# Optimization experiments

Hardware: AMD Instinct MI355X
Metric: run time of the kernel (lower is better)

## Reference

```python
import jax, jax.numpy as jnp
import numpy as np

B, T, DIM, H = 4, 2048, 512, 8
DECAY = 0.9

def setup_inputs():
    key = jax.random.key(0)
    ks = jax.random.split(key, 8)
    s = 1.0 / np.sqrt(DIM)
    def lin(k):
        return jax.random.normal(k, (DIM, DIM), jnp.float32) * s
    return {
        "q": jax.random.normal(ks[0], (B, T, DIM), jnp.float32),
        "k": jax.random.normal(ks[1], (B, T, DIM), jnp.float32),
        "v": jax.random.normal(ks[2], (B, T, DIM), jnp.float32),
        "Wa": lin(ks[3]), "ba": jnp.zeros((DIM,), jnp.float32),
        "Wb": lin(ks[4]), "bb": jnp.zeros((DIM,), jnp.float32),
        "Wg": lin(ks[5]), "bg": jnp.zeros((DIM,), jnp.float32),
        "Wo": lin(ks[6]), "bo": jnp.zeros((DIM,), jnp.float32),
    }

def _linear_scan(a, b):
    # h_t = a_t * h_{t-1} + b_t along time axis=1, via associative scan
    def combine(c1, c2):
        a1, b1 = c1
        a2, b2 = c2
        return a1 * a2, a2 * b1 + b2
    return jax.lax.associative_scan(combine, (a, b), axis=1)[1]

def reference(q, k, v, Wa, ba, Wb, bb, Wg, bg, Wo, bo):
    # --- Mamba-style selective scan on q (no residual) ---
    a = jax.nn.sigmoid(q @ Wa + ba)   # input-dependent decay [B,T,D]
    b = q @ Wb + bb                   # input injection       [B,T,D]
    h = _linear_scan(a, b)            # recurrent state       [B,T,D]
    g = jax.nn.sigmoid(q @ Wg + bg)   # gate
    m_out = (h * g) @ Wo + bo         # [B,T,D]

    # --- RetNet-style decay-weighted linear retention ---
    Dh = DIM // H
    qh = q.reshape(B, T, H, Dh)
    kh = k.reshape(B, T, H, Dh)
    vh = v.reshape(B, T, H, Dh)
    t = jnp.arange(T)
    delta = t[:, None] - t[None, :]           # t - s
    mask = delta >= 0                         # causal
    decay_mat = jnp.where(
        mask,
        jnp.exp(jnp.where(mask, delta, 0).astype(jnp.float32) * np.float32(np.log(DECAY))),
        0.0,
    )                                          # [T,T]
    scores = jnp.einsum('bthd,bshd->bhts', qh, kh) * decay_mat  # [B,H,T,T]
    r_out = jnp.einsum('bhts,bshd->bthd', scores, vh).reshape(B, T, DIM)

    return m_out + r_out
```

## Files before the change

kernel.cpp:

```cpp
#include <hip/hip_runtime.h>
#include <hip/hip_bf16.h>

typedef unsigned short u16;

#define BB 4
#define TT 2048
#define DIM 512
#define NH 8
#define DH 64
#define DECAY 0.9f

#define CC 64
#define NC 32
#define BHN 32

#define CHS 32
#define NSC 64

#define TM 128
#define TN 128
#define BK 64

#define SS 72

typedef __attribute__((ext_vector_type(8))) short bf16x8;
typedef __attribute__((ext_vector_type(4))) float f32x4;

__device__ __forceinline__ u16 f2bfu(float f) {
  union { float f; unsigned int u; } c; c.f = f;
  unsigned int u = c.u + 0x7FFFu + ((c.u >> 16) & 1u);
  return (u16)(u >> 16);
}
__device__ __forceinline__ float bf2f(u16 u) {
  union { unsigned int u; float f; } c; c.u = ((unsigned int)u) << 16;
  return c.f;
}

__device__ __forceinline__ void gl_lds16(const void* g, void* l) {
  __builtin_amdgcn_global_load_lds(
      (const __attribute__((address_space(1))) void*)g,
      (__attribute__((address_space(3))) void*)(unsigned int)(unsigned long long)l,
      16, 0, 0);
}

__device__ __forceinline__ void gemm_tile(
    int nTile, int mTile, const u16* __restrict__ A, const u16* __restrict__ Bt,
    const float* __restrict__ b0, const float* __restrict__ b1,
    const float* __restrict__ b2,
    u16* __restrict__ C0, u16* __restrict__ C1, u16* __restrict__ C2,
    int act_mask, u16* As, u16* Bs, int tid) {
  int wave = tid >> 6, lane = tid & 63;
  int group = (nTile * TN) >> 9;
  const float* bias = (group == 0) ? b0 : (group == 1) ? b1 : b2;
  u16* C = (group == 0) ? C0 : (group == 1) ? C1 : C2;
  int act = (act_mask >> group) & 1;

  int wm = (wave >> 1) * 64, wn = (wave & 1) * 64;
  int rowA = lane & 15, khalf = lane >> 4;

  f32x4 acc[4][4];
#pragma unroll
  for (int i = 0; i < 4; ++i)
#pragma unroll
    for (int j = 0; j < 4; ++j) acc[i][j] = (f32x4){0.f, 0.f, 0.f, 0.f};

  const u16* Abase = A + (size_t)mTile * TM * 512;
  const u16* Bbase = Bt + (size_t)nTile * TN * 512;

  for (int kk = 0; kk < 512; kk += BK) {
#pragma unroll
    for (int i = 0; i < 4; ++i) {
      int o = (wave * 4 + i) * 64 + lane;
      int row = o >> 3, gk = (o & 7) ^ (row & 7);
      gl_lds16(Abase + (size_t)row * 512 + kk + gk * 8, &As[o * 8]);
    }
#pragma unroll
    for (int i = 0; i < 4; ++i) {
      int o = (wave * 4 + i) * 64 + lane;
      int row = o >> 3, gk = (o & 7) ^ (row & 7);
      gl_lds16(Bbase + (size_t)row * 512 + kk + gk * 8, &Bs[o * 8]);
    }
    __syncthreads();
#pragma unroll
    for (int k0 = 0; k0 < 2; ++k0) {
      bf16x8 af[4], bfr[4];
#pragma unroll
      for (int mi = 0; mi < 4; ++mi) {
        int rr = wm + mi * 16 + rowA;
        int gk = k0 * 4 + khalf;
        int o = rr * 8 + (gk ^ (rr & 7));
        af[mi] = *(const bf16x8*)&As[o * 8];
      }
#pragma unroll
      for (int ni = 0; ni < 4; ++ni) {
        int rr = wn + ni * 16 + rowA;
        int gk = k0 * 4 + khalf;
        int o = rr * 8 + (gk ^ (rr & 7));
        bfr[ni] = *(const bf16x8*)&Bs[o * 8];
      }
#pragma unroll
      for (int mi = 0; mi < 4; ++mi)
#pragma unroll
        for (int ni = 0; ni < 4; ++ni)
          acc[mi][ni] = __builtin_amdgcn_mfma_f32_16x16x32_bf16(
              af[mi], bfr[ni], acc[mi][ni], 0, 0, 0);
    }
    __syncthreads();
  }
  int cloc = lane & 15, rq = (lane >> 4) * 4;
#pragma unroll
  for (int mi = 0; mi < 4; ++mi) {
#pragma unroll
    for (int r = 0; r < 4; ++r) {
      int m = mTile * TM + wm + mi * 16 + rq + r;
#pragma unroll
      for (int ni = 0; ni < 4; ++ni) {
        int n = (nTile * TN + wn + ni * 16 + cloc) & 511;
        float vv = acc[mi][ni][r] + bias[n];
        if (act) vv = 1.0f / (1.0f + __expf(-vv));
        C[(size_t)m * 512 + n] = f2bfu(vv);
      }
    }
  }
}

__device__ __forceinline__ void gemm_tile64(
    int nTile, int mTile, const u16* __restrict__ A, const u16* __restrict__ Bt,
    const float* __restrict__ bias, float* __restrict__ C,
    const u16* __restrict__ Radd, u16* As, u16* Bs, int tid) {
  int wave = tid >> 6, lane = tid & 63;
  int wm = wave * 32;
  int rowA = lane & 15, khalf = lane >> 4;

  f32x4 acc[2][4];
#pragma unroll
  for (int i = 0; i < 2; ++i)
#pragma unroll
    for (int j = 0; j < 4; ++j) acc[i][j] = (f32x4){0.f, 0.f, 0.f, 0.f};

  const u16* Abase = A + (size_t)mTile * TM * 512;
  const u16* Bbase = Bt + (size_t)nTile * 64 * 512;

  for (int kk = 0; kk < 512; kk += BK) {
#pragma unroll
    for (int i = 0; i < 4; ++i) {
      int o = (wave * 4 + i) * 64 + lane;
      int row = o >> 3, gk = (o & 7) ^ (row & 7);
      gl_lds16(Abase + (size_t)row * 512 + kk + gk * 8, &As[o * 8]);
    }
#pragma unroll
    for (int i = 0; i < 2; ++i) {
      int o = (wave * 2 + i) * 64 + lane;
      int row = o >> 3, gk = (o & 7) ^ (row & 7);
      gl_lds16(Bbase + (size_t)row * 512 + kk + gk * 8, &Bs[o * 8]);
    }
    __syncthreads();
#pragma unroll
    for (int k0 = 0; k0 < 2; ++k0) {
      bf16x8 af[2], bfr[4];
#pragma unroll
      for (int mi = 0; mi < 2; ++mi) {
        int rr = wm + mi * 16 + rowA;
        int gk = k0 * 4 + khalf;
        int o = rr * 8 + (gk ^ (rr & 7));
        af[mi] = *(const bf16x8*)&As[o * 8];
      }
#pragma unroll
      for (int ni = 0; ni < 4; ++ni) {
        int rr = ni * 16 + rowA;
        int gk = k0 * 4 + khalf;
        int o = rr * 8 + (gk ^ (rr & 7));
        bfr[ni] = *(const bf16x8*)&Bs[o * 8];
      }
#pragma unroll
      for (int mi = 0; mi < 2; ++mi)
#pragma unroll
        for (int ni = 0; ni < 4; ++ni)
          acc[mi][ni] = __builtin_amdgcn_mfma_f32_16x16x32_bf16(
              af[mi], bfr[ni], acc[mi][ni], 0, 0, 0);
    }
    __syncthreads();
  }
  int cloc = lane & 15, rq = (lane >> 4) * 4;
#pragma unroll
  for (int mi = 0; mi < 2; ++mi) {
#pragma unroll
    for (int r = 0; r < 4; ++r) {
      int m = mTile * TM + wm + mi * 16 + rq + r;
#pragma unroll
      for (int ni = 0; ni < 4; ++ni) {
        int n = nTile * 64 + ni * 16 + cloc;
        float vv = acc[mi][ni][r] + bias[n] + bf2f(Radd[(size_t)m * 512 + n]);
        C[(size_t)m * 512 + n] = vv;
      }
    }
  }
}

__global__ __launch_bounds__(256) void k1_prep(
    const float* __restrict__ q, u16* __restrict__ qbf,
    const float* __restrict__ W0, const float* __restrict__ W1,
    const float* __restrict__ W2, const float* __restrict__ W3,
    u16* __restrict__ Wt) {
  __shared__ float t[32][33];
  int bx = blockIdx.x, tid = threadIdx.x;
  if (bx < 1024) {
    int m = bx >> 8, rem = bx & 255;
    int n0 = (rem & 15) * 32, k0 = (rem >> 4) * 32;
    const float* W = (m == 0) ? W0 : (m == 1) ? W1 : (m == 2) ? W2 : W3;
    int tx = tid & 31, ty = tid >> 5;
#pragma unroll
    for (int r = 0; r < 32; r += 8)
      t[ty + r][tx] = W[(size_t)(k0 + ty + r) * DIM + n0 + tx];
    __syncthreads();
    u16* o = Wt + (size_t)m * DIM * DIM;
#pragma unroll
    for (int r = 0; r < 32; r += 8)
      o[(size_t)(n0 + ty + r) * DIM + k0 + tx] = f2bfu(t[tx][ty + r]);
  } else {
    int i = (bx - 1024) * 256 + tid;
    float4 f = ((const float4*)q)[i];
    ushort4 u;
    u.x = f2bfu(f.x); u.y = f2bfu(f.y); u.z = f2bfu(f.z); u.w = f2bfu(f.w);
    ((ushort4*)qbf)[i] = u;
  }
}

__global__ __launch_bounds__(256) void k2_gemmab_retkv(
    const u16* __restrict__ qbf, const u16* __restrict__ WtAll,
    const float* __restrict__ ba, const float* __restrict__ bb,
    const float* __restrict__ bg,
    u16* __restrict__ Ab16, u16* __restrict__ Bb16, u16* __restrict__ Gb16,
    const float* __restrict__ k, const float* __restrict__ v,
    u16* __restrict__ KVTb, u16* __restrict__ VTg) {
  __shared__ __align__(16) u16 smem[TM * BK + TN * BK];
  int bx = blockIdx.x, tid = threadIdx.x;
  if (bx < 512) {
    gemm_tile(bx & 7, bx >> 3, qbf, WtAll, ba, bb, bg, Ab16, Bb16, Gb16,
              0b101, smem, smem + TM * BK, tid);
    return;
  }
  int idx = bx - 512;
  int bh = idx & 31, c = idx >> 5;
  int b = bh >> 3, h = bh & 7;
  int wave = tid >> 6, lane = tid & 63;
  u16* VT = smem;
  u16* KT = smem + 64 * SS;
  size_t base = ((size_t)(b * TT + c * CC)) * DIM + h * DH;
  int row = tid >> 2, part = tid & 3, e0 = part * 16;
  float w = __powf(DECAY, (float)(63 - row));
  {
    const float4* vs = (const float4*)(v + base + (size_t)row * DIM + e0);
    const float4* ks = (const float4*)(k + base + (size_t)row * DIM + e0);
#pragma unroll
    for (int u4 = 0; u4 < 4; ++u4) {
      float4 fv = vs[u4], fk = ks[u4];
      VT[(e0 + u4 * 4 + 0) * SS + row] = f2bfu(fv.x);
      VT[(e0 + u4 * 4 + 1) * SS + row] = f2bfu(fv.y);
      VT[(e0 + u4 * 4 + 2) * SS + row] = f2bfu(fv.z);
      VT[(e0 + u4 * 4 + 3) * SS + row] = f2bfu(fv.w);
      KT[(e0 + u4 * 4 + 0) * SS + row] = f2bfu(fk.x * w);
      KT[(e0 + u4 * 4 + 1) * SS + row] = f2bfu(fk.y * w);
      KT[(e0 + u4 * 4 + 2) * SS + row] = f2bfu(fk.z * w);
      KT[(e0 + u4 * 4 + 3) * SS + row] = f2bfu(fk.w * w);
    }
  }
  __syncthreads();
  {
    int e = row;
    u16* dst = VTg + ((size_t)bh * 64 + e) * TT + c * 64 + part * 16;
    *(uint4*)dst = *(const uint4*)&VT[e * SS + part * 16];
    *(uint4*)(dst + 8) = *(const uint4*)&VT[e * SS + part * 16 + 8];
  }
  int wm = (wave >> 1) * 32, wn = (wave & 1) * 32;
  int rowA = lane & 15, khalf = lane >> 4;
  f32x4 acc[2][2];
#pragma unroll
  for (int i = 0; i < 2; ++i)
#pragma unroll
    for (int j = 0; j < 2; ++j) acc[i][j] = (f32x4){0.f, 0.f, 0.f, 0.f};
#pragma unroll
  for (int k0 = 0; k0 < 2; ++k0) {
    int gk = k0 * 4 + khalf;
    bf16x8 af[2], bfr[2];
#pragma unroll
    for (int mi = 0; mi < 2; ++mi)
      af[mi] = *(const bf16x8*)&VT[(wm + mi * 16 + rowA) * SS + gk * 8];
#pragma unroll
    for (int ni = 0; ni < 2; ++ni)
      bfr[ni] = *(const bf16x8*)&KT[(wn + ni * 16 + rowA) * SS + gk * 8];
#pragma unroll
    for (int mi = 0; mi < 2; ++mi)
#pragma unroll
      for (int ni = 0; ni < 2; ++ni)
        acc[mi][ni] = __builtin_amdgcn_mfma_f32_16x16x32_bf16(
            af[mi], bfr[ni], acc[mi][ni], 0, 0, 0);
  }
  int cloc = lane & 15, rq = (lane >> 4) * 4;
  u16* o = KVTb + ((size_t)(c * BHN + bh)) * 4096;
#pragma unroll
  for (int mi = 0; mi < 2; ++mi)
#pragma unroll
    for (int r = 0; r < 4; ++r) {
      int e = wm + mi * 16 + rq + r;
#pragma unroll
      for (int ni = 0; ni < 2; ++ni)
        o[e * 64 + (wn + ni * 16 + cloc)] = f2bfu(acc[mi][ni][r]);
    }
}

__global__ __launch_bounds__(256) void k3_gemmg_part_retscan(
    const u16* __restrict__ qbf, const u16* __restrict__ WtAll,
    const float* __restrict__ ba, const float* __restrict__ bb,
    const float* __restrict__ bg,
    u16* __restrict__ Ab16, u16* __restrict__ Bb16, u16* __restrict__ Gb16,
    float* __restrict__ SA, float* __restrict__ SB,
    const u16* __restrict__ KVTb, u16* __restrict__ Ptb) {
  __shared__ __align__(16) u16 smem[TM * BK + TN * BK];
  int bx = blockIdx.x, tid = threadIdx.x;
  if (bx < 256) {
    gemm_tile(8 + (bx & 3), bx >> 2, qbf, WtAll, ba, bb, bg, Ab16, Bb16, Gb16,
              0b101, smem, smem + TM * BK, tid);
  } else if (bx < 768) {
    int bxx = bx - 256;
    int ci = bxx >> 3, grp = bxx & 7;
    int ch = grp * 256 + tid;
    int bb2 = ch >> 9, d = ch & 511;
    size_t base = ((size_t)bb2 * TT + ci * CHS) * DIM + d;
    float h = 0.f, pA = 1.f;
#pragma unroll
    for (int t = 0; t < CHS; ++t) {
      float av = bf2f(Ab16[base + (size_t)t * DIM]);
      float bv = bf2f(Bb16[base + (size_t)t * DIM]);
      h = fmaf(av, h, bv);
      pA *= av;
    }
    SA[ci * 2048 + ch] = pA;
    SB[ci * 2048 + ch] = h;
  } else {
    int gid = (bx - 768) * 256 + tid;
    int bh = gid >> 12, ed = gid & 4095;
    float carry = 0.f;
    const float dC = __powf(DECAY, (float)CC);
    for (int c = 0; c < NC; ++c) {
      size_t idx = ((size_t)(c * BHN + bh)) * 4096 + ed;
      Ptb[idx] = f2bfu(carry);
      carry = fmaf(dC, carry, bf2f(KVTb[idx]));
    }
  }
}

__global__ __launch_bounds__(256) void k4_apply_retout(
    const u16* __restrict__ Ab16, const u16* __restrict__ Bb16,
    const u16* __restrict__ g, const float* __restrict__ SA,
    const float* __restrict__ SB, u16* __restrict__ hg,
    const u16* __restrict__ qbf, const float* __restrict__ kg,
    const u16* __restrict__ VTg, const u16* __restrict__ Ptb,
    u16* __restrict__ routb) {
  __shared__ __align__(16) u16 Sa[64 * SS];
  __shared__ float dp[66];
  int bx = blockIdx.x, tid = threadIdx.x;
  if (bx < 512) {
    int ci = bx >> 3, grp = bx & 7;
    int ch = grp * 256 + tid;
    int bb = ch >> 9, d = ch & 511;
    float carry = 0.f;
    for (int p = 0; p < ci; ++p)
      carry = fmaf(SA[p * 2048 + ch], carry, SB[p * 2048 + ch]);
    size_t base = ((size_t)bb * TT + ci * CHS) * DIM + d;
    float h = carry;
#pragma unroll
    for (int t = 0; t < CHS; ++t) {
      size_t idx = base + (size_t)t * DIM;
      h = fmaf(bf2f(Ab16[idx]), h, bf2f(Bb16[idx]));
      hg[idx] = f2bfu(h * bf2f(g[idx]));
    }
    return;
  }
  int idx2 = bx - 512;
  int bh = idx2 & 31, c = idx2 >> 5;
  int b = bh >> 3, h = bh & 7;
  int wave = tid >> 6, lane = tid & 63;
  size_t base = ((size_t)(b * TT + c * CC)) * DIM + h * DH;
  if (tid < 66) dp[tid] = __powf(DECAY, (float)tid);

  int wm = (wave >> 1) * 32, wn = (wave & 1) * 32;
  int rowA = lane & 15, khalf = lane >> 4;

  bf16x8 afq[2][2];
#pragma unroll
  for (int k0 = 0; k0 < 2; ++k0)
#pragma unroll
    for (int mi = 0; mi < 2; ++mi)
      afq[k0][mi] = *(const bf16x8*)(qbf + base +
          (size_t)(wm + mi * 16 + rowA) * 512 + (k0 * 4 + khalf) * 8);
  bf16x8 bfk[2][2];
#pragma unroll
  for (int k0 = 0; k0 < 2; ++k0)
#pragma unroll
    for (int ni = 0; ni < 2; ++ni) {
      const float* kp = kg + base + (size_t)(wn + ni * 16 + rowA) * 512 +
                        (k0 * 4 + khalf) * 8;
      float4 f0 = *(const float4*)kp;
      float4 f1 = *(const float4*)(kp + 4);
      bf16x8 t;
      t[0] = (short)f2bfu(f0.x); t[1] = (short)f2bfu(f0.y);
      t[2] = (short)f2bfu(f0.z); t[3] = (short)f2bfu(f0.w);
      t[4] = (short)f2bfu(f1.x); t[5] = (short)f2bfu(f1.y);
      t[6] = (short)f2bfu(f1.z); t[7] = (short)f2bfu(f1.w);
      bfk[k0][ni] = t;
    }

  f32x4 accS[2][2];
#pragma unroll
  for (int i = 0; i < 2; ++i)
#pragma unroll
    for (int j = 0; j < 2; ++j) accS[i][j] = (f32x4){0.f, 0.f, 0.f, 0.f};
#pragma unroll
  for (int k0 = 0; k0 < 2; ++k0)
#pragma unroll
    for (int mi = 0; mi < 2; ++mi)
#pragma unroll
      for (int ni = 0; ni < 2; ++ni)
        accS[mi][ni] = __builtin_amdgcn_mfma_f32_16x16x32_bf16(
            afq[k0][mi], bfk[k0][ni], accS[mi][ni], 0, 0, 0);
  __syncthreads();

  int cloc = lane & 15, rq = (lane >> 4) * 4;
#pragma unroll
  for (int mi = 0; mi < 2; ++mi)
#pragma unroll
    for (int ni = 0; ni < 2; ++ni)
#pragma unroll
      for (int r = 0; r < 4; ++r) {
        int i = wm + mi * 16 + rq + r;
        int j = wn + ni * 16 + cloc;
        float sv = (j <= i) ? accS[mi][ni][r] * dp[i - j] : 0.f;
        Sa[i * SS + j] = f2bfu(sv);
      }
#pragma unroll
  for (int mi = 0; mi < 2; ++mi) {
    float s = dp[wm + mi * 16 + rowA + 1];
#pragma unroll
    for (int k0 = 0; k0 < 2; ++k0) {
      bf16x8 t = afq[k0][mi];
#pragma unroll
      for (int u = 0; u < 8; ++u)
        t[u] = (short)f2bfu(bf2f((u16)t[u]) * s);
      afq[k0][mi] = t;
    }
  }
  __syncthreads();

  f32x4 accO[2][2];
#pragma unroll
  for (int i = 0; i < 2; ++i)
#pragma unroll
    for (int j = 0; j < 2; ++j) accO[i][j] = (f32x4){0.f, 0.f, 0.f, 0.f};
#pragma unroll
  for (int k0 = 0; k0 < 4; ++k0) {
    bf16x8 af[2], bfv[2];
#pragma unroll
    for (int mi = 0; mi < 2; ++mi) {
      if (k0 < 2)
        af[mi] = *(const bf16x8*)&Sa[(wm + mi * 16 + rowA) * SS +
                                     (k0 * 4 + khalf) * 8];
      else
        af[mi] = afq[k0 - 2][mi];
    }
#pragma unroll
    for (int ni = 0; ni < 2; ++ni) {
      int e = wn + ni * 16 + rowA;
      if (k0 < 2)
        bfv[ni] = *(const bf16x8*)(VTg + ((size_t)bh * 64 + e) * TT + c * 64 +
                                   (k0 * 4 + khalf) * 8);
      else
        bfv[ni] = *(const bf16x8*)(Ptb + ((size_t)(c * BHN + bh)) * 4096 +
                                   e * 64 + ((k0 - 2) * 4 + khalf) * 8);
    }
#pragma unroll
    for (int mi = 0; mi < 2; ++mi)
#pragma unroll
      for (int ni = 0; ni < 2; ++ni)
        accO[mi][ni] = __builtin_amdgcn_mfma_f32_16x16x32_bf16(
            af[mi], bfv[ni], accO[mi][ni], 0, 0, 0);
  }
#pragma unroll
  for (int mi = 0; mi < 2; ++mi)
#pragma unroll
    for (int r = 0; r < 4; ++r) {
      int i = wm + mi * 16 + rq + r;
#pragma unroll
      for (int ni = 0; ni < 2; ++ni) {
        int e = wn + ni * 16 + cloc;
        routb[base + (size_t)i * 512 + e] = f2bfu(accO[mi][ni][r]);
      }
    }
}

__global__ __launch_bounds__(256) void k5_gemm2(
    const u16* __restrict__ hgbf, const u16* __restrict__ Wto,
    const float* __restrict__ bo, float* __restrict__ out,
    const u16* __restrict__ routb) {
  __shared__ __align__(16) u16 smem[TM * BK + 64 * BK];
  gemm_tile64(blockIdx.x & 7, blockIdx.x >> 3, hgbf, Wto, bo, out, routb,
              smem, smem + TM * BK, threadIdx.x);
}

extern "C" void kernel_launch(void* const* d_in, const int* in_sizes, int n_in,
                              void* d_out, int out_size, void* d_ws, size_t ws_size,
                              hipStream_t stream) {
  const float* q  = (const float*)d_in[0];
  const float* k  = (const float*)d_in[1];
  const float* v  = (const float*)d_in[2];
  const float* Wa = (const float*)d_in[3];
  const float* ba = (const float*)d_in[4];
  const float* Wb = (const float*)d_in[5];
  const float* bb = (const float*)d_in[6];
  const float* Wg = (const float*)d_in[7];
  const float* bg = (const float*)d_in[8];
  const float* Wo = (const float*)d_in[9];
  const float* bo = (const float*)d_in[10];
  float* out = (float*)d_out;
  float* ws = (float*)d_ws;

  const size_t NEL = (size_t)BB * TT * DIM;
  float* SA = ws;
  float* SB = SA + NSC * 2048;
  u16* up = (u16*)(SB + NSC * 2048);
  u16* Ab16  = up;  up += NEL;
  u16* Bb16  = up;  up += NEL;
  u16* Gb16  = up;  up += NEL;
  u16* qbf   = up;  up += NEL;
  u16* hgbf  = up;  up += NEL;
  u16* WtAll = up;  up += 4 * DIM * DIM;
  u16* KVTb  = up;  up += (size_t)NC * BHN * 4096;
  u16* Ptb   = up;  up += (size_t)NC * BHN * 4096;
  u16* VTg   = up;  up += (size_t)BHN * 64 * TT;
  u16* routb = up;  up += NEL;

  k1_prep<<<5120, 256, 0, stream>>>(q, qbf, Wa, Wb, Wg, Wo, WtAll);

  k2_gemmab_retkv<<<1536, 256, 0, stream>>>(qbf, WtAll, ba, bb, bg,
                                            Ab16, Bb16, Gb16, k, v, KVTb, VTg);

  k3_gemmg_part_retscan<<<1280, 256, 0, stream>>>(qbf, WtAll, ba, bb, bg,
                                                  Ab16, Bb16, Gb16,
                                                  SA, SB, KVTb, Ptb);

  k4_apply_retout<<<1536, 256, 0, stream>>>(Ab16, Bb16, Gb16, SA, SB, hgbf,
                                            qbf, k, VTg, Ptb, routb);

  k5_gemm2<<<512, 256, 0, stream>>>(hgbf, WtAll + 3 * DIM * DIM,
                                    bo, out, routb);
}
```

Before: 185.4 us.

## Regroup kernel stages: move retention KV into prep, merge all projection GEMMs

Moves the per-chunk retention K^T V computation into the prep kernel, where it runs alongside weight transposes and q conversion. All three projection GEMM tile sets (A, B, G) now go in a single launch together with the retention carry scan. The chunk-partial selective-scan pass is split out into its own small kernel. The aim is better load balance and fewer dependency bubbles between launches. The cost is a larger shared memory footprint in the prep kernel, which may reduce its occupancy.

```diff
diff --git a/kernel.cpp b/kernel.cpp
--- a/kernel.cpp
+++ b/kernel.cpp
@@ -197,15 +197,86 @@
   }
 }
 
-__global__ __launch_bounds__(256) void k1_prep(
+__global__ __launch_bounds__(256) void k1_prep_retkv(
     const float* __restrict__ q, u16* __restrict__ qbf,
     const float* __restrict__ W0, const float* __restrict__ W1,
     const float* __restrict__ W2, const float* __restrict__ W3,
-    u16* __restrict__ Wt) {
+    u16* __restrict__ Wt,
+    const float* __restrict__ k, const float* __restrict__ v,
+    u16* __restrict__ KVTb, u16* __restrict__ VTg) {
+  __shared__ __align__(16) u16 smem[2 * 64 * SS];
   __shared__ float t[32][33];
   int bx = blockIdx.x, tid = threadIdx.x;
   if (bx < 1024) {
-    int m = bx >> 8, rem = bx & 255;
+    int bh = bx & 31, c = bx >> 5;
+    int b = bh >> 3, h = bh & 7;
+    int wave = tid >> 6, lane = tid & 63;
+    u16* VT = smem;
+    u16* KT = smem + 64 * SS;
+    size_t base = ((size_t)(b * TT + c * CC)) * DIM + h * DH;
+    int row = tid >> 2, part = tid & 3, e0 = part * 16;
+    float w = __powf(DECAY, (float)(63 - row));
+    {
+      const float4* vs = (const float4*)(v + base + (size_t)row * DIM + e0);
+      const float4* ks = (const float4*)(k + base + (size_t)row * DIM + e0);
+#pragma unroll
+      for (int u4 = 0; u4 < 4; ++u4) {
+        float4 fv = vs[u4], fk = ks[u4];
+        VT[(e0 + u4 * 4 + 0) * SS + row] = f2bfu(fv.x);
+        VT[(e0 + u4 * 4 + 1) * SS + row] = f2bfu(fv.y);
+        VT[(e0 + u4 * 4 + 2) * SS + row] = f2bfu(fv.z);
+        VT[(e0 + u4 * 4 + 3) * SS + row] = f2bfu(fv.w);
+        KT[(e0 + u4 * 4 + 0) * SS + row] = f2bfu(fk.x * w);
+        KT[(e0 + u4 * 4 + 1) * SS + row] = f2bfu(fk.y * w);
+        KT[(e0 + u4 * 4 + 2) * SS + row] = f2bfu(fk.z * w);
+        KT[(e0 + u4 * 4 + 3) * SS + row] = f2bfu(fk.w * w);
+      }
+    }
+    __syncthreads();
+    {
+      int e = row;
+      u16* dst = VTg + ((size_t)bh * 64 + e) * TT + c * 64 + part * 16;
+      *(uint4*)dst = *(const uint4*)&VT[e * SS + part * 16];
+      *(uint4*)(dst + 8) = *(const uint4*)&VT[e * SS + part * 16 + 8];
+    }
+    int wm = (wave >> 1) * 32, wn = (wave & 1) * 32;
+    int rowA = lane & 15, khalf = lane >> 4;
+    f32x4 acc[2][2];
+#pragma unroll
+    for (int i = 0; i < 2; ++i)
+#pragma unroll
+      for (int j = 0; j < 2; ++j) acc[i][j] = (f32x4){0.f, 0.f, 0.f, 0.f};
+#pragma unroll
+    for (int k0 = 0; k0 < 2; ++k0) {
+      int gk = k0 * 4 + khalf;
+      bf16x8 af[2], bfr[2];
+#pragma unroll
+      for (int mi = 0; mi < 2; ++mi)
+        af[mi] = *(const bf16x8*)&VT[(wm + mi * 16 + rowA) * SS + gk * 8];
+#pragma unroll
+      for (int ni = 0; ni < 2; ++ni)
+        bfr[ni] = *(const bf16x8*)&KT[(wn + ni * 16 + rowA) * SS + gk * 8];
+#pragma unroll
+      for (int mi = 0; mi < 2; ++mi)
+#pragma unroll
+        for (int ni = 0; ni < 2; ++ni)
+          acc[mi][ni] = __builtin_amdgcn_mfma_f32_16x16x32_bf16(
+              af[mi], bfr[ni], acc[mi][ni], 0, 0, 0);
+    }
+    int cloc = lane & 15, rq = (lane >> 4) * 4;
+    u16* o = KVTb + ((size_t)(c * BHN + bh)) * 4096;
+#pragma unroll
+    for (int mi = 0; mi < 2; ++mi)
+#pragma unroll
+      for (int r = 0; r < 4; ++r) {
+        int e = wm + mi * 16 + rq + r;
+#pragma unroll
+        for (int ni = 0; ni < 2; ++ni)
+          o[e * 64 + (wn + ni * 16 + cloc)] = f2bfu(acc[mi][ni][r]);
+      }
+  } else if (bx < 2048) {
+    int bx2 = bx - 1024;
+    int m = bx2 >> 8, rem = bx2 & 255;
     int n0 = (rem & 15) * 32, k0 = (rem >> 4) * 32;
     const float* W = (m == 0) ? W0 : (m == 1) ? W1 : (m == 2) ? W2 : W3;
     int tx = tid & 31, ty = tid >> 5;
@@ -218,7 +289,7 @@
     for (int r = 0; r < 32; r += 8)
       o[(size_t)(n0 + ty + r) * DIM + k0 + tx] = f2bfu(t[tx][ty + r]);
   } else {
-    int i = (bx - 1024) * 256 + tid;
+    int i = (bx - 2048) * 256 + tid;
     float4 f = ((const float4*)q)[i];
     ushort4 u;
     u.x = f2bfu(f.x); u.y = f2bfu(f.y); u.z = f2bfu(f.z); u.w = f2bfu(f.w);
@@ -226,117 +297,17 @@
   }
 }
 
-__global__ __launch_bounds__(256) void k2_gemmab_retkv(
+__global__ __launch_bounds__(256) void k2_gemm1_retscan(
     const u16* __restrict__ qbf, const u16* __restrict__ WtAll,
     const float* __restrict__ ba, const float* __restrict__ bb,
     const float* __restrict__ bg,
     u16* __restrict__ Ab16, u16* __restrict__ Bb16, u16* __restrict__ Gb16,
-    const float* __restrict__ k, const float* __restrict__ v,
-    u16* __restrict__ KVTb, u16* __restrict__ VTg) {
-  __shared__ __align__(16) u16 smem[TM * BK + TN * BK];
-  int bx = blockIdx.x, tid = threadIdx.x;
-  if (bx < 512) {
-    gemm_tile(bx & 7, bx >> 3, qbf, WtAll, ba, bb, bg, Ab16, Bb16, Gb16,
-              0b101, smem, smem + TM * BK, tid);
-    return;
-  }
-  int idx = bx - 512;
-  int bh = idx & 31, c = idx >> 5;
-  int b = bh >> 3, h = bh & 7;
-  int wave = tid >> 6, lane = tid & 63;
-  u16* VT = smem;
-  u16* KT = smem + 64 * SS;
-  size_t base = ((size_t)(b * TT + c * CC)) * DIM + h * DH;
-  int row = tid >> 2, part = tid & 3, e0 = part * 16;
-  float w = __powf(DECAY, (float)(63 - row));
-  {
-    const float4* vs = (const float4*)(v + base + (size_t)row * DIM + e0);
-    const float4* ks = (const float4*)(k + base + (size_t)row * DIM + e0);
-#pragma unroll
-    for (int u4 = 0; u4 < 4; ++u4) {
-      float4 fv = vs[u4], fk = ks[u4];
-      VT[(e0 + u4 * 4 + 0) * SS + row] = f2bfu(fv.x);
-      VT[(e0 + u4 * 4 + 1) * SS + row] = f2bfu(fv.y);
-      VT[(e0 + u4 * 4 + 2) * SS + row] = f2bfu(fv.z);
-      VT[(e0 + u4 * 4 + 3) * SS + row] = f2bfu(fv.w);
-      KT[(e0 + u4 * 4 + 0) * SS + row] = f2bfu(fk.x * w);
-      KT[(e0 + u4 * 4 + 1) * SS + row] = f2bfu(fk.y * w);
-      KT[(e0 + u4 * 4 + 2) * SS + row] = f2bfu(fk.z * w);
-      KT[(e0 + u4 * 4 + 3) * SS + row] = f2bfu(fk.w * w);
-    }
-  }
-  __syncthreads();
-  {
-    int e = row;
-    u16* dst = VTg + ((size_t)bh * 64 + e) * TT + c * 64 + part * 16;
-    *(uint4*)dst = *(const uint4*)&VT[e * SS + part * 16];
-    *(uint4*)(dst + 8) = *(const uint4*)&VT[e * SS + part * 16 + 8];
-  }
-  int wm = (wave >> 1) * 32, wn = (wave & 1) * 32;
-  int rowA = lane & 15, khalf = lane >> 4;
-  f32x4 acc[2][2];
-#pragma unroll
-  for (int i = 0; i < 2; ++i)
-#pragma unroll
-    for (int j = 0; j < 2; ++j) acc[i][j] = (f32x4){0.f, 0.f, 0.f, 0.f};
-#pragma unroll
-  for (int k0 = 0; k0 < 2; ++k0) {
-    int gk = k0 * 4 + khalf;
-    bf16x8 af[2], bfr[2];
-#pragma unroll
-    for (int mi = 0; mi < 2; ++mi)
-      af[mi] = *(const bf16x8*)&VT[(wm + mi * 16 + rowA) * SS + gk * 8];
-#pragma unroll
-    for (int ni = 0; ni < 2; ++ni)
-      bfr[ni] = *(const bf16x8*)&KT[(wn + ni * 16 + rowA) * SS + gk * 8];
-#pragma unroll
-    for (int mi = 0; mi < 2; ++mi)
-#pragma unroll
-      for (int ni = 0; ni < 2; ++ni)
-        acc[mi][ni] = __builtin_amdgcn_mfma_f32_16x16x32_bf16(
-            af[mi], bfr[ni], acc[mi][ni], 0, 0, 0);
-  }
-  int cloc = lane & 15, rq = (lane >> 4) * 4;
-  u16* o = KVTb + ((size_t)(c * BHN + bh)) * 4096;
-#pragma unroll
-  for (int mi = 0; mi < 2; ++mi)
-#pragma unroll
-    for (int r = 0; r < 4; ++r) {
-      int e = wm + mi * 16 + rq + r;
-#pragma unroll
-      for (int ni = 0; ni < 2; ++ni)
-        o[e * 64 + (wn + ni * 16 + cloc)] = f2bfu(acc[mi][ni][r]);
-    }
-}
-
-__global__ __launch_bounds__(256) void k3_gemmg_part_retscan(
-    const u16* __restrict__ qbf, const u16* __restrict__ WtAll,
-    const float* __restrict__ ba, const float* __restrict__ bb,
-    const float* __restrict__ bg,
-    u16* __restrict__ Ab16, u16* __restrict__ Bb16, u16* __restrict__ Gb16,
-    float* __restrict__ SA, float* __restrict__ SB,
     const u16* __restrict__ KVTb, u16* __restrict__ Ptb) {
   __shared__ __align__(16) u16 smem[TM * BK + TN * BK];
   int bx = blockIdx.x, tid = threadIdx.x;
-  if (bx < 256) {
-    gemm_tile(8 + (bx & 3), bx >> 2, qbf, WtAll, ba, bb, bg, Ab16, Bb16, Gb16,
+  if (bx < 768) {
+    gemm_tile(bx % 12, bx / 12, qbf, WtAll, ba, bb, bg, Ab16, Bb16, Gb16,
               0b101, smem, smem + TM * BK, tid);
-  } else if (bx < 768) {
-    int bxx = bx - 256;
-    int ci = bxx >> 3, grp = bxx & 7;
-    int ch = grp * 256 + tid;
-    int bb2 = ch >> 9, d = ch & 511;
-    size_t base = ((size_t)bb2 * TT + ci * CHS) * DIM + d;
-    float h = 0.f, pA = 1.f;
-#pragma unroll
-    for (int t = 0; t < CHS; ++t) {
-      float av = bf2f(Ab16[base + (size_t)t * DIM]);
-      float bv = bf2f(Bb16[base + (size_t)t * DIM]);
-      h = fmaf(av, h, bv);
-      pA *= av;
-    }
-    SA[ci * 2048 + ch] = pA;
-    SB[ci * 2048 + ch] = h;
   } else {
     int gid = (bx - 768) * 256 + tid;
     int bh = gid >> 12, ed = gid & 4095;
@@ -348,6 +319,24 @@
       carry = fmaf(dC, carry, bf2f(KVTb[idx]));
     }
   }
+}
+
+__global__ void k3_part(const u16* __restrict__ Ab16, const u16* __restrict__ Bb16,
+                        float* __restrict__ SA, float* __restrict__ SB) {
+  int ci = blockIdx.x >> 3, grp = blockIdx.x & 7;
+  int ch = grp * 256 + threadIdx.x;
+  int bb2 = ch >> 9, d = ch & 511;
+  size_t base = ((size_t)bb2 * TT + ci * CHS) * DIM + d;
+  float h = 0.f, pA = 1.f;
+#pragma unroll
+  for (int t = 0; t < CHS; ++t) {
+    float av = bf2f(Ab16[base + (size_t)t * DIM]);
+    float bv = bf2f(Bb16[base + (size_t)t * DIM]);
+    h = fmaf(av, h, bv);
+    pA *= av;
+  }
+  SA[ci * 2048 + ch] = pA;
+  SB[ci * 2048 + ch] = h;
 }
 
 __global__ __launch_bounds__(256) void k4_apply_retout(
@@ -539,14 +528,13 @@
   u16* VTg   = up;  up += (size_t)BHN * 64 * TT;
   u16* routb = up;  up += NEL;
 
-  k1_prep<<<5120, 256, 0, stream>>>(q, qbf, Wa, Wb, Wg, Wo, WtAll);
-
-  k2_gemmab_retkv<<<1536, 256, 0, stream>>>(qbf, WtAll, ba, bb, bg,
-                                            Ab16, Bb16, Gb16, k, v, KVTb, VTg);
-
-  k3_gemmg_part_retscan<<<1280, 256, 0, stream>>>(qbf, WtAll, ba, bb, bg,
-                                                  Ab16, Bb16, Gb16,
-                                                  SA, SB, KVTb, Ptb);
+  k1_prep_retkv<<<6144, 256, 0, stream>>>(q, qbf, Wa, Wb, Wg, Wo, WtAll,
+                                          k, v, KVTb, VTg);
+
+  k2_gemm1_retscan<<<1280, 256, 0, stream>>>(qbf, WtAll, ba, bb, bg,
+                                             Ab16, Bb16, Gb16, KVTb, Ptb);
+
+  k3_part<<<512, 256, 0, stream>>>(Ab16, Bb16, SA, SB);
 
   k4_apply_retout<<<1536, 256, 0, stream>>>(Ab16, Bb16, Gb16, SA, SB, hgbf,
                                             qbf, k, VTg, Ptb, routb);
```

Result: faster. 174.6 us (-5.8%).
